# Kernel tuning notes

Measured on AMD Instinct MI355X. Metric: run time of the kernel, lower is better.

Reference implementation:

```python
import jax, jax.numpy as jnp
import numpy as np
import math

D_MODEL = 1024
N_HEADS = 16
D_K = D_MODEL // N_HEADS
D_FF = 4096
B, S = 4, 2048
EPS = 1e-5


def layer_norm(x, scale, bias):
    mu = jnp.mean(x, axis=-1, keepdims=True)
    var = jnp.mean(jnp.square(x - mu), axis=-1, keepdims=True)
    return (x - mu) * jax.lax.rsqrt(var + EPS) * scale + bias


def setup_inputs() -> dict:
    key = jax.random.key(0)
    ks = jax.random.split(key, 16)
    init = lambda k, shape, fan_in: jax.random.normal(k, shape, jnp.float32) / np.sqrt(fan_in)
    x = jax.random.normal(ks[0], (B, S, D_MODEL), jnp.float32)
    # causal mask: positions where mask==0 are blocked
    mask = jnp.tril(jnp.ones((S, S), dtype=bool))[None, None, :, :]
    return {
        "x": x,
        "mask": mask,
        "wq": init(ks[1], (D_MODEL, D_MODEL), D_MODEL), "bq": jnp.zeros((D_MODEL,), jnp.float32),
        "wk": init(ks[2], (D_MODEL, D_MODEL), D_MODEL), "bk": jnp.zeros((D_MODEL,), jnp.float32),
        "wv": init(ks[3], (D_MODEL, D_MODEL), D_MODEL), "bv": jnp.zeros((D_MODEL,), jnp.float32),
        "wo": init(ks[4], (D_MODEL, D_MODEL), D_MODEL), "bo": jnp.zeros((D_MODEL,), jnp.float32),
        "w1": init(ks[5], (D_FF, D_MODEL), D_MODEL), "b1": jnp.zeros((D_FF,), jnp.float32),
        "w2": init(ks[6], (D_MODEL, D_FF), D_FF), "b2": jnp.zeros((D_MODEL,), jnp.float32),
        "ln1_s": jnp.ones((D_MODEL,), jnp.float32), "ln1_b": jnp.zeros((D_MODEL,), jnp.float32),
        "ln2_s": jnp.ones((D_MODEL,), jnp.float32), "ln2_b": jnp.zeros((D_MODEL,), jnp.float32),
    }


def reference(x, mask, wq, bq, wk, bk, wv, bv, wo, bo, w1, b1, w2, b2, ln1_s, ln1_b, ln2_s, ln2_b):
    b, s, _ = x.shape
    # projections (torch Linear: y = x @ W.T + b); split heads -> [b, h, s, d_k]
    def proj(w, bias):
        return (jnp.einsum('bsd,ed->bse', x, w) + bias).reshape(b, s, N_HEADS, D_K).transpose(0, 2, 1, 3)
    Q, K, V = proj(wq, bq), proj(wk, bk), proj(wv, bv)
    scores = jnp.einsum('bhqd,bhkd->bhqk', Q, K) / math.sqrt(D_K)  # [b,h,s,s]
    scores = jnp.where(mask, scores, jnp.float32(-1e9))
    attn = jax.nn.softmax(scores, axis=-1)
    ctx = jnp.einsum('bhqk,bhkd->bhqd', attn, V)
    ctx = ctx.transpose(0, 2, 1, 3).reshape(b, s, D_MODEL)
    attn_out = jnp.einsum('bsd,ed->bse', ctx, wo) + bo
    h = layer_norm(x + attn_out, ln1_s, ln1_b)
    ff = jnp.einsum('bsd,fd->bsf', h, w1) + b1
    ff = jax.nn.gelu(ff, approximate=False)
    ff = jnp.einsum('bsf,df->bsd', ff, w2) + b2
    return layer_norm(h + ff, ln2_s, ln2_b)
```

## Files before the change

kernel.cpp:

```cpp
#include <hip/hip_runtime.h>
#include <hip/hip_bf16.h>
#include <math.h>

using bf16 = __hip_bfloat16;
using bf16x8 = __attribute__((ext_vector_type(8))) short;
using f32x4 = __attribute__((ext_vector_type(4))) float;

#define D_MODEL 1024
#define N_HEADS 16
#define D_K 64
#define D_FF 4096
#define BATCH 4
#define SEQ 2048
#define M_TOT (BATCH*SEQ)

__device__ __forceinline__ void async_copy16(void* lds, const void* g) {
    __builtin_amdgcn_global_load_lds((const __attribute__((address_space(1))) void*)g,
                                     (__attribute__((address_space(3))) void*)lds, 16, 0, 0);
}

__global__ void __launch_bounds__(256) cvt_kernel(const float* __restrict__ src,
                                                  bf16* __restrict__ dst, int n) {
    int nchunk = n >> 2;
    int stride = gridDim.x * blockDim.x;
    for (int i = blockIdx.x * blockDim.x + threadIdx.x; i < nchunk; i += stride) {
        float4 v = *(const float4*)&src[i * 4];
        union { bf16 h[4]; short4 s; } u;
        u.h[0] = __float2bfloat16(v.x);
        u.h[1] = __float2bfloat16(v.y);
        u.h[2] = __float2bfloat16(v.z);
        u.h[3] = __float2bfloat16(v.w);
        *(short4*)&dst[i * 4] = u.s;
    }
}

template<int EPI>
__global__ void __launch_bounds__(256) gemm_bt(const bf16* __restrict__ A,
                                               const bf16* __restrict__ B,
                                               const float* __restrict__ bias,
                                               const float* __restrict__ resid,
                                               float* __restrict__ Cf,
                                               bf16* __restrict__ Cb,
                                               int M, int N, int K) {
    __shared__ __align__(16) bf16 As[128 * 32];
    __shared__ __align__(16) bf16 Bs[128 * 32];
    const int tid  = threadIdx.x;
    const int lane = tid & 63;
    const int wave = tid >> 6;
    const int quad = lane >> 4;
    const int l16  = lane & 15;
    const int wr   = (wave >> 1) * 64;
    const int wc   = (wave & 1) * 64;
    const int m0   = blockIdx.y * 128;
    const int n0   = blockIdx.x * 128;

    const bf16* Ag = A + (size_t)m0 * K;
    const bf16* Bg = B + (size_t)n0 * K;

    f32x4 acc[4][4] = {};

    for (int k0 = 0; k0 < K; k0 += 32) {
        __syncthreads();
#pragma unroll
        for (int p = 0; p < 2; p++) {
            int c = p * 256 + tid;
            int row = c >> 2;
            int col = (c & 3) << 3;
            async_copy16(&As[c * 8], Ag + (size_t)row * K + k0 + col);
            async_copy16(&Bs[c * 8], Bg + (size_t)row * K + k0 + col);
        }
        __syncthreads();
        bf16x8 a[4], b[4];
#pragma unroll
        for (int i = 0; i < 4; i++)
            a[i] = *(const bf16x8*)&As[(wr + i * 16 + l16) * 32 + quad * 8];
#pragma unroll
        for (int j = 0; j < 4; j++)
            b[j] = *(const bf16x8*)&Bs[(wc + j * 16 + l16) * 32 + quad * 8];
#pragma unroll
        for (int i = 0; i < 4; i++)
#pragma unroll
            for (int j = 0; j < 4; j++)
                acc[i][j] = __builtin_amdgcn_mfma_f32_16x16x32_bf16(a[i], b[j], acc[i][j], 0, 0, 0);
    }

#pragma unroll
    for (int i = 0; i < 4; i++) {
#pragma unroll
        for (int r = 0; r < 4; r++) {
            int row = m0 + wr + i * 16 + quad * 4 + r;
            size_t rb = (size_t)row * N;
#pragma unroll
            for (int j = 0; j < 4; j++) {
                int col = n0 + wc + j * 16 + l16;
                float v = acc[i][j][r] + bias[col];
                if (EPI == 0) {
                    Cb[rb + col] = __float2bfloat16(v);
                } else if (EPI == 1) {
                    Cf[rb + col] = v + resid[rb + col];
                } else if (EPI == 2) {
                    float g = 0.5f * v * (1.0f + erff(v * 0.70710678118654752f));
                    Cb[rb + col] = __float2bfloat16(g);
                } else {
                    float sc = (col < 1024) ? 0.18033688011112043f : 1.0f;
                    Cb[rb + col] = __float2bfloat16(v * sc);
                }
            }
        }
    }
}

__global__ void __launch_bounds__(256) attn_kernel(const bf16* __restrict__ qkv,
                                                   bf16* __restrict__ ctx) {
    const int qb   = (int)gridDim.x - 1 - (int)blockIdx.x;
    const int h    = blockIdx.y;
    const int bb   = blockIdx.z;
    const int tid  = threadIdx.x;
    const int lane = tid & 63;
    const int wave = tid >> 6;
    const int quad = lane >> 4;
    const int l16  = lane & 15;

    __shared__ __align__(16) bf16 Pool[4 * 32 * 80];
    __shared__ __align__(16) bf16 Ks[64 * 64];
    __shared__ __align__(16) bf16 Vt[64 * 80];

    const size_t rowbase = (size_t)(bb * SEQ) * 3072;
    const int q0 = qb * 128;

#pragma unroll
    for (int p = 0; p < 4; p++) {
        int c = p * 256 + tid;
        int row = c >> 3;
        int off = (c & 7) * 8;
        async_copy16(&Pool[c * 8], qkv + rowbase + (size_t)(q0 + row) * 3072 + h * 64 + off);
    }
    __syncthreads();

    bf16x8 aq[2][2];
#pragma unroll
    for (int i = 0; i < 2; i++)
#pragma unroll
        for (int kd = 0; kd < 2; kd++)
            aq[i][kd] = *(const bf16x8*)&Pool[(wave * 32 + i * 16 + l16) * 64 + kd * 32 + quad * 8];

    f32x4 o[2][4] = {};
    float l_acc[2][4] = {};

    bf16* Pw = &Pool[wave * 32 * 80];
    const int swkey = (l16 >> 2) & 3;

    const int nkb = 2 * (qb + 1);
    for (int kb = 0; kb < nkb; kb++) {
        __syncthreads();
#pragma unroll
        for (int p = 0; p < 2; p++) {
            int c = p * 256 + tid;
            int row = c >> 3;
            int off = (c & 7) * 8;
            async_copy16(&Ks[c * 8],
                         qkv + rowbase + (size_t)(kb * 64 + row) * 3072 + 1024 + h * 64 + off);
        }
#pragma unroll
        for (int it = 0; it < 2; it++) {
            int c = it * 256 + tid;
            int k = c & 63;
            int d0 = (c >> 6) * 8;
            bf16x8 v = *(const bf16x8*)&qkv[rowbase + (size_t)(kb * 64 + k) * 3072 + 2048 + h * 64 + d0];
#pragma unroll
            for (int u = 0; u < 8; u++)
                Vt[(d0 + u) * 80 + k] = ((const bf16*)&v)[u];
        }
        __syncthreads();

        f32x4 s[2][4] = {};
#pragma unroll
        for (int jb = 0; jb < 4; jb++) {
#pragma unroll
            for (int kd = 0; kd < 2; kd++) {
                bf16x8 bk = *(const bf16x8*)&Ks[(jb * 16 + l16) * 64 + kd * 32 + quad * 8];
#pragma unroll
                for (int i = 0; i < 2; i++)
                    s[i][jb] = __builtin_amdgcn_mfma_f32_16x16x32_bf16(aq[i][kd], bk, s[i][jb], 0, 0, 0);
            }
        }

        const bool diagb = (kb >= 2 * qb);
#pragma unroll
        for (int i = 0; i < 2; i++) {
            const int row0 = q0 + wave * 32 + i * 16;
            const bool needmask = diagb && (kb * 64 + 63 > row0);
#pragma unroll
            for (int jb = 0; jb < 4; jb++) {
                const int colg = kb * 64 + jb * 16 + l16;
                const int colsw = ((jb ^ quad) * 16) + l16;
#pragma unroll
                for (int r = 0; r < 4; r++) {
                    float t = s[i][jb][r];
                    if (needmask && colg > row0 + quad * 4 + r) t = -1e30f;
                    float p = exp2f(t);
                    l_acc[i][r] += p;
                    Pw[(i * 16 + quad * 4 + r) * 80 + colsw] = __float2bfloat16(p);
                }
            }
        }

#pragma unroll
        for (int kk = 0; kk < 2; kk++) {
            bf16x8 bv[4];
#pragma unroll
            for (int nb = 0; nb < 4; nb++)
                bv[nb] = *(const bf16x8*)&Vt[(nb * 16 + l16) * 80 + kk * 32 + quad * 8];
            const int grp = kk * 2 + (quad >> 1);
            const int coff = ((grp ^ swkey) * 16) + (quad & 1) * 8;
#pragma unroll
            for (int i = 0; i < 2; i++) {
                bf16x8 ap = *(const bf16x8*)&Pw[(i * 16 + l16) * 80 + coff];
#pragma unroll
                for (int nb = 0; nb < 4; nb++)
                    o[i][nb] = __builtin_amdgcn_mfma_f32_16x16x32_bf16(ap, bv[nb], o[i][nb], 0, 0, 0);
            }
        }
    }

#pragma unroll
    for (int i = 0; i < 2; i++)
#pragma unroll
        for (int r = 0; r < 4; r++) {
#pragma unroll
            for (int msk = 1; msk < 16; msk <<= 1)
                l_acc[i][r] += __shfl_xor(l_acc[i][r], msk, 64);
        }

#pragma unroll
    for (int i = 0; i < 2; i++)
#pragma unroll
        for (int r = 0; r < 4; r++) {
            int rowg = q0 + wave * 32 + i * 16 + quad * 4 + r;
            size_t base = ((size_t)(bb * SEQ + rowg)) * D_MODEL + h * 64;
            float inv = 1.0f / l_acc[i][r];
#pragma unroll
            for (int nb = 0; nb < 4; nb++)
                ctx[base + nb * 16 + l16] = __float2bfloat16(o[i][nb][r] * inv);
        }
}

__global__ void __launch_bounds__(256) ln_kernel(const float* __restrict__ in,
                                                 const float* __restrict__ sc,
                                                 const float* __restrict__ bi,
                                                 float* __restrict__ of,
                                                 bf16* __restrict__ ob) {
    int row = blockIdx.x;
    const float* rp = in + (size_t)row * D_MODEL;
    int t = threadIdx.x;
    float4 v = *(const float4*)&rp[t * 4];
    float s1 = v.x + v.y + v.z + v.w;
    float s2 = v.x * v.x + v.y * v.y + v.z * v.z + v.w * v.w;
#pragma unroll
    for (int m = 32; m > 0; m >>= 1) {
        s1 += __shfl_xor(s1, m, 64);
        s2 += __shfl_xor(s2, m, 64);
    }
    __shared__ float red[8];
    int wave = t >> 6, lane = t & 63;
    if (lane == 0) { red[wave] = s1; red[wave + 4] = s2; }
    __syncthreads();
    float S1 = red[0] + red[1] + red[2] + red[3];
    float S2 = red[4] + red[5] + red[6] + red[7];
    float mu = S1 * (1.0f / 1024.0f);
    float var = S2 * (1.0f / 1024.0f) - mu * mu;
    float rstd = rsqrtf(var + 1e-5f);
    float4 g = *(const float4*)&sc[t * 4];
    float4 b = *(const float4*)&bi[t * 4];
    float o0 = (v.x - mu) * rstd * g.x + b.x;
    float o1 = (v.y - mu) * rstd * g.y + b.y;
    float o2 = (v.z - mu) * rstd * g.z + b.z;
    float o3 = (v.w - mu) * rstd * g.w + b.w;
    size_t base = (size_t)row * D_MODEL + t * 4;
    if (of) {
        float4 ov; ov.x = o0; ov.y = o1; ov.z = o2; ov.w = o3;
        *(float4*)&of[base] = ov;
    }
    if (ob) {
        union { bf16 h[4]; short4 s; } u;
        u.h[0] = __float2bfloat16(o0);
        u.h[1] = __float2bfloat16(o1);
        u.h[2] = __float2bfloat16(o2);
        u.h[3] = __float2bfloat16(o3);
        *(short4*)&ob[base] = u.s;
    }
}

static const size_t OFF_WQKV = 0;
static const size_t OFF_WO   = 6291456;
static const size_t OFF_W1   = 8388608;
static const size_t OFF_W2   = 16777216;
static const size_t OFF_BQKV = 25165824;
static const size_t OFF_XB   = 25178112;
static const size_t OFF_QKV  = 41955328;
static const size_t OFF_CTX  = 92286976;
static const size_t OFF_HF   = 109064192;
static const size_t OFF_HB   = 142618624;
static const size_t OFF_FF   = 159395840;
static const size_t OFF_RES1 = OFF_QKV;
static const size_t OFF_RES2 = OFF_XB;

extern "C" void kernel_launch(void* const* d_in, const int* in_sizes, int n_in,
                              void* d_out, int out_size, void* d_ws, size_t ws_size,
                              hipStream_t stream) {
    const float* x     = (const float*)d_in[0];
    const float* wq    = (const float*)d_in[2];
    const float* bq    = (const float*)d_in[3];
    const float* wk    = (const float*)d_in[4];
    const float* bk    = (const float*)d_in[5];
    const float* wv    = (const float*)d_in[6];
    const float* bv    = (const float*)d_in[7];
    const float* wo    = (const float*)d_in[8];
    const float* bo    = (const float*)d_in[9];
    const float* w1    = (const float*)d_in[10];
    const float* b1    = (const float*)d_in[11];
    const float* w2    = (const float*)d_in[12];
    const float* b2    = (const float*)d_in[13];
    const float* ln1_s = (const float*)d_in[14];
    const float* ln1_b = (const float*)d_in[15];
    const float* ln2_s = (const float*)d_in[16];
    const float* ln2_b = (const float*)d_in[17];

    char* ws = (char*)d_ws;
    bf16* wqkv_b = (bf16*)(ws + OFF_WQKV);
    bf16* wo_b   = (bf16*)(ws + OFF_WO);
    bf16* w1_b   = (bf16*)(ws + OFF_W1);
    bf16* w2_b   = (bf16*)(ws + OFF_W2);
    float* bqkv  = (float*)(ws + OFF_BQKV);
    bf16* x_b    = (bf16*)(ws + OFF_XB);
    bf16* qkv    = (bf16*)(ws + OFF_QKV);
    bf16* ctx    = (bf16*)(ws + OFF_CTX);
    float* h_f   = (float*)(ws + OFF_HF);
    bf16* h_b    = (bf16*)(ws + OFF_HB);
    bf16* ff     = (bf16*)(ws + OFF_FF);
    float* res1  = (float*)(ws + OFF_RES1);
    float* res2  = (float*)(ws + OFF_RES2);

    cvt_kernel<<<1024, 256, 0, stream>>>(wq, wqkv_b, 1024 * 1024);
    cvt_kernel<<<1024, 256, 0, stream>>>(wk, wqkv_b + 1024 * 1024, 1024 * 1024);
    cvt_kernel<<<1024, 256, 0, stream>>>(wv, wqkv_b + 2 * 1024 * 1024, 1024 * 1024);
    cvt_kernel<<<1024, 256, 0, stream>>>(wo, wo_b, 1024 * 1024);
    cvt_kernel<<<2048, 256, 0, stream>>>(w1, w1_b, 4096 * 1024);
    cvt_kernel<<<2048, 256, 0, stream>>>(w2, w2_b, 4096 * 1024);
    cvt_kernel<<<2048, 256, 0, stream>>>(x, x_b, M_TOT * D_MODEL);
    hipMemcpyAsync(bqkv,        bq, 1024 * sizeof(float), hipMemcpyDeviceToDevice, stream);
    hipMemcpyAsync(bqkv + 1024, bk, 1024 * sizeof(float), hipMemcpyDeviceToDevice, stream);
    hipMemcpyAsync(bqkv + 2048, bv, 1024 * sizeof(float), hipMemcpyDeviceToDevice, stream);

    gemm_bt<3><<<dim3(3072 / 128, M_TOT / 128), 256, 0, stream>>>(
        x_b, wqkv_b, bqkv, nullptr, nullptr, qkv, M_TOT, 3072, 1024);

    attn_kernel<<<dim3(SEQ / 128, N_HEADS, BATCH), 256, 0, stream>>>(qkv, ctx);

    gemm_bt<1><<<dim3(1024 / 128, M_TOT / 128), 256, 0, stream>>>(
        ctx, wo_b, bo, x, res1, nullptr, M_TOT, 1024, 1024);

    ln_kernel<<<M_TOT, 256, 0, stream>>>(res1, ln1_s, ln1_b, h_f, h_b);

    gemm_bt<2><<<dim3(4096 / 128, M_TOT / 128), 256, 0, stream>>>(
        h_b, w1_b, b1, nullptr, nullptr, ff, M_TOT, 4096, 1024);

    gemm_bt<1><<<dim3(1024 / 128, M_TOT / 128), 256, 0, stream>>>(
        ff, w2_b, b2, h_f, res2, nullptr, M_TOT, 1024, 4096);

    ln_kernel<<<M_TOT, 256, 0, stream>>>(res2, ln2_s, ln2_b, (float*)d_out, nullptr);
}
```

Baseline: 720.8 us.

## Pair causal query blocks per workgroup and double-buffer K/V tiles in attention

```diff
diff --git a/kernel.cpp b/kernel.cpp
--- a/kernel.cpp
+++ b/kernel.cpp
@@ -112,7 +112,7 @@
 
 __global__ void __launch_bounds__(256) attn_kernel(const bf16* __restrict__ qkv,
                                                    bf16* __restrict__ ctx) {
-    const int qb   = (int)gridDim.x - 1 - (int)blockIdx.x;
+    const int pair = blockIdx.x;
     const int h    = blockIdx.y;
     const int bb   = blockIdx.z;
     const int tid  = threadIdx.x;
@@ -122,127 +122,156 @@
     const int l16  = lane & 15;
 
     __shared__ __align__(16) bf16 Pool[4 * 32 * 80];
-    __shared__ __align__(16) bf16 Ks[64 * 64];
-    __shared__ __align__(16) bf16 Vt[64 * 80];
+    __shared__ __align__(16) bf16 Ks[2][64 * 64];
+    __shared__ __align__(16) bf16 Vt[2][64 * 80];
 
     const size_t rowbase = (size_t)(bb * SEQ) * 3072;
-    const int q0 = qb * 128;
-
-#pragma unroll
-    for (int p = 0; p < 4; p++) {
-        int c = p * 256 + tid;
-        int row = c >> 3;
-        int off = (c & 7) * 8;
-        async_copy16(&Pool[c * 8], qkv + rowbase + (size_t)(q0 + row) * 3072 + h * 64 + off);
-    }
-    __syncthreads();
-
-    bf16x8 aq[2][2];
-#pragma unroll
-    for (int i = 0; i < 2; i++)
-#pragma unroll
-        for (int kd = 0; kd < 2; kd++)
-            aq[i][kd] = *(const bf16x8*)&Pool[(wave * 32 + i * 16 + l16) * 64 + kd * 32 + quad * 8];
-
-    f32x4 o[2][4] = {};
-    float l_acc[2][4] = {};
-
     bf16* Pw = &Pool[wave * 32 * 80];
     const int swkey = (l16 >> 2) & 3;
 
-    const int nkb = 2 * (qb + 1);
-    for (int kb = 0; kb < nkb; kb++) {
+#pragma unroll 1
+    for (int phase = 0; phase < 2; phase++) {
+        const int qb = (phase == 0) ? pair : (15 - pair);
+        const int q0 = qb * 128;
+        const int nkb = 2 * (qb + 1);
+
         __syncthreads();
-#pragma unroll
-        for (int p = 0; p < 2; p++) {
+
+#pragma unroll
+        for (int p = 0; p < 4; p++) {
             int c = p * 256 + tid;
             int row = c >> 3;
             int off = (c & 7) * 8;
-            async_copy16(&Ks[c * 8],
-                         qkv + rowbase + (size_t)(kb * 64 + row) * 3072 + 1024 + h * 64 + off);
-        }
-#pragma unroll
-        for (int it = 0; it < 2; it++) {
-            int c = it * 256 + tid;
-            int k = c & 63;
-            int d0 = (c >> 6) * 8;
-            bf16x8 v = *(const bf16x8*)&qkv[rowbase + (size_t)(kb * 64 + k) * 3072 + 2048 + h * 64 + d0];
-#pragma unroll
-            for (int u = 0; u < 8; u++)
-                Vt[(d0 + u) * 80 + k] = ((const bf16*)&v)[u];
-        }
+            async_copy16(&Pool[c * 8], qkv + rowbase + (size_t)(q0 + row) * 3072 + h * 64 + off);
+        }
+#pragma unroll
+        for (int p = 0; p < 2; p++) {
+            int c = p * 256 + tid;
+            async_copy16(&Ks[0][c * 8],
+                         qkv + rowbase + (size_t)(c >> 3) * 3072 + 1024 + h * 64 + (c & 7) * 8);
+        }
+        const int vk  = tid & 63;
+        const int vd0a = (tid >> 6) * 8;
+        const int vd0b = vd0a + 32;
+        bf16x8 vr0 = *(const bf16x8*)&qkv[rowbase + (size_t)vk * 3072 + 2048 + h * 64 + vd0a];
+        bf16x8 vr1 = *(const bf16x8*)&qkv[rowbase + (size_t)vk * 3072 + 2048 + h * 64 + vd0b];
+
         __syncthreads();
 
-        f32x4 s[2][4] = {};
-#pragma unroll
-        for (int jb = 0; jb < 4; jb++) {
-#pragma unroll
-            for (int kd = 0; kd < 2; kd++) {
-                bf16x8 bk = *(const bf16x8*)&Ks[(jb * 16 + l16) * 64 + kd * 32 + quad * 8];
-#pragma unroll
-                for (int i = 0; i < 2; i++)
-                    s[i][jb] = __builtin_amdgcn_mfma_f32_16x16x32_bf16(aq[i][kd], bk, s[i][jb], 0, 0, 0);
-            }
-        }
-
-        const bool diagb = (kb >= 2 * qb);
-#pragma unroll
-        for (int i = 0; i < 2; i++) {
-            const int row0 = q0 + wave * 32 + i * 16;
-            const bool needmask = diagb && (kb * 64 + 63 > row0);
+        bf16x8 aq[2][2];
+#pragma unroll
+        for (int i = 0; i < 2; i++)
+#pragma unroll
+            for (int kd = 0; kd < 2; kd++)
+                aq[i][kd] = *(const bf16x8*)&Pool[(wave * 32 + i * 16 + l16) * 64 + kd * 32 + quad * 8];
+
+#pragma unroll
+        for (int u = 0; u < 8; u++) {
+            Vt[0][(vd0a + u) * 80 + vk] = ((const bf16*)&vr0)[u];
+            Vt[0][(vd0b + u) * 80 + vk] = ((const bf16*)&vr1)[u];
+        }
+
+        f32x4 o[2][4] = {};
+        float l_acc[2][4] = {};
+
+#pragma unroll 1
+        for (int kb = 0; kb < nkb; kb++) {
+            const int cur = kb & 1;
+            const int nxt = cur ^ 1;
+            __syncthreads();
+
+            const bool pf = (kb + 1 < nkb);
+            bf16x8 nv0, nv1;
+            if (pf) {
+#pragma unroll
+                for (int p = 0; p < 2; p++) {
+                    int c = p * 256 + tid;
+                    async_copy16(&Ks[nxt][c * 8],
+                                 qkv + rowbase + (size_t)((kb + 1) * 64 + (c >> 3)) * 3072 + 1024 + h * 64 + (c & 7) * 8);
+                }
+                nv0 = *(const bf16x8*)&qkv[rowbase + (size_t)((kb + 1) * 64 + vk) * 3072 + 2048 + h * 64 + vd0a];
+                nv1 = *(const bf16x8*)&qkv[rowbase + (size_t)((kb + 1) * 64 + vk) * 3072 + 2048 + h * 64 + vd0b];
+            }
+
+            f32x4 s[2][4] = {};
 #pragma unroll
             for (int jb = 0; jb < 4; jb++) {
-                const int colg = kb * 64 + jb * 16 + l16;
-                const int colsw = ((jb ^ quad) * 16) + l16;
-#pragma unroll
-                for (int r = 0; r < 4; r++) {
-                    float t = s[i][jb][r];
-                    if (needmask && colg > row0 + quad * 4 + r) t = -1e30f;
-                    float p = exp2f(t);
-                    l_acc[i][r] += p;
-                    Pw[(i * 16 + quad * 4 + r) * 80 + colsw] = __float2bfloat16(p);
-                }
-            }
-        }
-
-#pragma unroll
-        for (int kk = 0; kk < 2; kk++) {
-            bf16x8 bv[4];
-#pragma unroll
-            for (int nb = 0; nb < 4; nb++)
-                bv[nb] = *(const bf16x8*)&Vt[(nb * 16 + l16) * 80 + kk * 32 + quad * 8];
-            const int grp = kk * 2 + (quad >> 1);
-            const int coff = ((grp ^ swkey) * 16) + (quad & 1) * 8;
+#pragma unroll
+                for (int kd = 0; kd < 2; kd++) {
+                    bf16x8 bk = *(const bf16x8*)&Ks[cur][(jb * 16 + l16) * 64 + kd * 32 + quad * 8];
+#pragma unroll
+                    for (int i = 0; i < 2; i++)
+                        s[i][jb] = __builtin_amdgcn_mfma_f32_16x16x32_bf16(aq[i][kd], bk, s[i][jb], 0, 0, 0);
+                }
+            }
+
+            if (pf) {
+#pragma unroll
+                for (int u = 0; u < 8; u++) {
+                    Vt[nxt][(vd0a + u) * 80 + vk] = ((const bf16*)&nv0)[u];
+                    Vt[nxt][(vd0b + u) * 80 + vk] = ((const bf16*)&nv1)[u];
+                }
+            }
+
+            const bool diagb = (kb >= 2 * qb);
 #pragma unroll
             for (int i = 0; i < 2; i++) {
-                bf16x8 ap = *(const bf16x8*)&Pw[(i * 16 + l16) * 80 + coff];
+                const int row0 = q0 + wave * 32 + i * 16;
+                const bool needmask = diagb && (kb * 64 + 63 > row0);
+#pragma unroll
+                for (int jb = 0; jb < 4; jb++) {
+                    const int colg = kb * 64 + jb * 16 + l16;
+                    const int colsw = ((jb ^ quad) * 16) + l16;
+#pragma unroll
+                    for (int r = 0; r < 4; r++) {
+                        float t = s[i][jb][r];
+                        if (needmask && colg > row0 + quad * 4 + r) t = -1e30f;
+                        float p = exp2f(t);
+                        l_acc[i][r] += p;
+                        Pw[(i * 16 + quad * 4 + r) * 80 + colsw] = __float2bfloat16(p);
+                    }
+                }
+            }
+
+#pragma unroll
+            for (int kk = 0; kk < 2; kk++) {
+                bf16x8 bv[4];
 #pragma unroll
                 for (int nb = 0; nb < 4; nb++)
-                    o[i][nb] = __builtin_amdgcn_mfma_f32_16x16x32_bf16(ap, bv[nb], o[i][nb], 0, 0, 0);
-            }
-        }
-    }
-
-#pragma unroll
-    for (int i = 0; i < 2; i++)
-#pragma unroll
-        for (int r = 0; r < 4; r++) {
-#pragma unroll
-            for (int msk = 1; msk < 16; msk <<= 1)
-                l_acc[i][r] += __shfl_xor(l_acc[i][r], msk, 64);
-        }
-
-#pragma unroll
-    for (int i = 0; i < 2; i++)
-#pragma unroll
-        for (int r = 0; r < 4; r++) {
-            int rowg = q0 + wave * 32 + i * 16 + quad * 4 + r;
-            size_t base = ((size_t)(bb * SEQ + rowg)) * D_MODEL + h * 64;
-            float inv = 1.0f / l_acc[i][r];
-#pragma unroll
-            for (int nb = 0; nb < 4; nb++)
-                ctx[base + nb * 16 + l16] = __float2bfloat16(o[i][nb][r] * inv);
-        }
+                    bv[nb] = *(const bf16x8*)&Vt[cur][(nb * 16 + l16) * 80 + kk * 32 + quad * 8];
+                const int grp = kk * 2 + (quad >> 1);
+                const int coff = ((grp ^ swkey) * 16) + (quad & 1) * 8;
+#pragma unroll
+                for (int i = 0; i < 2; i++) {
+                    bf16x8 ap = *(const bf16x8*)&Pw[(i * 16 + l16) * 80 + coff];
+#pragma unroll
+                    for (int nb = 0; nb < 4; nb++)
+                        o[i][nb] = __builtin_amdgcn_mfma_f32_16x16x32_bf16(ap, bv[nb], o[i][nb], 0, 0, 0);
+                }
+            }
+        }
+
+#pragma unroll
+        for (int i = 0; i < 2; i++)
+#pragma unroll
+            for (int r = 0; r < 4; r++) {
+#pragma unroll
+                for (int msk = 1; msk < 16; msk <<= 1)
+                    l_acc[i][r] += __shfl_xor(l_acc[i][r], msk, 64);
+            }
+
+#pragma unroll
+        for (int i = 0; i < 2; i++)
+#pragma unroll
+            for (int r = 0; r < 4; r++) {
+                int rowg = q0 + wave * 32 + i * 16 + quad * 4 + r;
+                size_t base = ((size_t)(bb * SEQ + rowg)) * D_MODEL + h * 64;
+                float inv = 1.0f / l_acc[i][r];
+#pragma unroll
+                for (int nb = 0; nb < 4; nb++)
+                    ctx[base + nb * 16 + l16] = __float2bfloat16(o[i][nb][r] * inv);
+            }
+    }
 }
 
 __global__ void __launch_bounds__(256) ln_kernel(const float* __restrict__ in,
@@ -355,7 +384,7 @@
     gemm_bt<3><<<dim3(3072 / 128, M_TOT / 128), 256, 0, stream>>>(
         x_b, wqkv_b, bqkv, nullptr, nullptr, qkv, M_TOT, 3072, 1024);
 
-    attn_kernel<<<dim3(SEQ / 128, N_HEADS, BATCH), 256, 0, stream>>>(qkv, ctx);
+    attn_kernel<<<dim3(8, N_HEADS, BATCH), 256, 0, stream>>>(qkv, ctx);
 
     gemm_bt<1><<<dim3(1024 / 128, M_TOT / 128), 256, 0, stream>>>(
         ctx, wo_b, bo, x, res1, nullptr, M_TOT, 1024, 1024);
```

Result: faster. 652.9 us (-9.4%).
